# Optimization experiments

Hardware: AMD Instinct MI355X
Metric: run time of the kernel (lower is better)

## Reference

```python
import jax, jax.numpy as jnp
import numpy as np

B, S, D_IN = 32, 128, 17
D_PT, D_PAIR, D_OUT = 64, 128, 64
EPS = 1e-5


def _gelu(x):
    return jax.nn.gelu(x, approximate=False)  # torch nn.GELU default (erf)


def _bn(h, g, b):
    # BatchNorm1d (training mode): stats over batch and pair dims, per channel
    mean = h.mean(axis=(0, 1))
    var = h.var(axis=(0, 1))  # biased, matching torch normalization
    return (h - mean) * jax.lax.rsqrt(var + EPS) * g + b


def setup_inputs() -> dict:
    key = jax.random.key(0)
    ks = jax.random.split(key, 8)
    s = lambda k, shp, fan: jax.random.normal(k, shp, jnp.float32) * (1.0 / np.sqrt(fan))
    return {
        "x": jax.random.normal(ks[0], (B, S, D_IN), jnp.float32),
        # pointwise MLP: 17 -> 64 -> 64
        "w1": s(ks[1], (D_IN, D_PT), D_IN), "b1": jnp.zeros((D_PT,), jnp.float32),
        "w2": s(ks[2], (D_PT, D_PT), D_PT), "b2": jnp.zeros((D_PT,), jnp.float32),
        # pair MLP: 128 -> 128 -> 128 (input = 2 * D_PT)
        "wp1": s(ks[3], (2 * D_PT, D_PAIR), 2 * D_PT), "bp1": jnp.zeros((D_PAIR,), jnp.float32),
        "wp2": s(ks[4], (D_PAIR, D_PAIR), D_PAIR), "bp2": jnp.zeros((D_PAIR,), jnp.float32),
        # embed: BN(128) -> Conv1d(128,64,1) -> BN(64) -> GELU -> Conv1d(64,64,1) -> BN(64)
        "g0": jnp.ones((D_PAIR,), jnp.float32), "be0": jnp.zeros((D_PAIR,), jnp.float32),
        "wc1": s(ks[5], (D_PAIR, D_OUT), D_PAIR), "bc1": jnp.zeros((D_OUT,), jnp.float32),
        "g1": jnp.ones((D_OUT,), jnp.float32), "be1": jnp.zeros((D_OUT,), jnp.float32),
        "wc2": s(ks[6], (D_OUT, D_OUT), D_OUT), "bc2": jnp.zeros((D_OUT,), jnp.float32),
        "g2": jnp.ones((D_OUT,), jnp.float32), "be2": jnp.zeros((D_OUT,), jnp.float32),
    }


def reference(x, w1, b1, w2, b2, wp1, bp1, wp2, bp2,
              g0, be0, wc1, bc1, g1, be1, wc2, bc2, g2, be2):
    seq_len = x.shape[1]
    # pointwise MLP
    h = _gelu(x @ w1 + b1)
    h = _gelu(h @ w2 + b2)  # [B, S, D_PT]
    # tril pair gather (xi = features of particle j, xj = of particle i,
    # matching x_rep[b, a, c] = x[b, c] semantics in the torch code)
    i_idx, j_idx = jnp.tril_indices(seq_len)
    xi = h[:, j_idx, :]  # [B, P, D_PT]
    xj = h[:, i_idx, :]
    xij = jnp.concatenate([xi, xj], axis=-1)  # [B, P, 2*D_PT]
    # pair MLP
    e = _gelu(xij @ wp1 + bp1)
    e = _gelu(e @ wp2 + bp2)  # [B, P, D_PAIR]
    # embed stack (Conv1d k=1 == channel-wise linear)
    e = _bn(e, g0, be0)
    e = _gelu(_bn(e @ wc1 + bc1, g1, be1))
    e = _bn(e @ wc2 + bc2, g2, be2)  # [B, P, D_OUT]
    # symmetric scatter into dense pairwise output
    y = jnp.zeros((x.shape[0], seq_len, seq_len, e.shape[-1]), e.dtype)
    y = y.at[:, i_idx, j_idx, :].set(e)
    y = y.at[:, j_idx, i_idx, :].set(e)
    return y
```

## Files before the change

### kernel.cpp

```cpp
#include <hip/hip_runtime.h>
#include <hip/hip_bf16.h>
#include <math.h>

#define BB 32
#define SS 128
#define DIN 17
#define DPT 64
#define DPA 128
#define DOU 64
#define NP 8256
#define NROWS (BB * NP)
#define NCHUNK (NROWS / 128)
#define EPSF 1e-5f

typedef __hip_bfloat16 bf16;
typedef __attribute__((ext_vector_type(8))) short short8;
typedef __attribute__((ext_vector_type(16))) float f32x16;
typedef __attribute__((ext_vector_type(4))) float f32x4;
typedef __attribute__((ext_vector_type(4))) int int4v;

#define MFMA32(a, b, c) __builtin_amdgcn_mfma_f32_32x32x16_bf16(a, b, c, 0, 0, 0)

__device__ __forceinline__ unsigned short bfb(float f) {
    return __builtin_bit_cast(unsigned short, __float2bfloat16(f));
}
__device__ __forceinline__ float bf2f(short u) {
    return __builtin_bit_cast(float, ((unsigned int)(unsigned short)u) << 16);
}

__device__ __forceinline__ float gelu_exact(float x) {
    float z = fabsf(x) * 0.7071067811865476f;
    float t = __builtin_amdgcn_rcpf(fmaf(0.3275911f, z, 1.0f));
    float p = fmaf(t, 1.061405429f, -1.453152027f);
    p = fmaf(t, p, 1.421413741f);
    p = fmaf(t, p, -0.284496736f);
    p = fmaf(t, p, 0.254829592f);
    p *= t;
    float e = __expf(-z * z);
    float erfz = 1.0f - p * e;
    float s = copysignf(erfz, x);
    return 0.5f * x * (1.0f + s);
}

__global__ void k_pairs(int* __restrict__ pairIJ) {
    int p = blockIdx.x * blockDim.x + threadIdx.x;
    if (p >= NP) return;
    int i = (int)((sqrtf(8.0f * (float)p + 1.0f) - 1.0f) * 0.5f);
    while ((i * (i + 1)) / 2 > p) --i;
    while (((i + 1) * (i + 2)) / 2 <= p) ++i;
    int j = p - (i * (i + 1)) / 2;
    pairIJ[p] = (i << 8) | j;
}

__global__ void k_pack(const float* __restrict__ wp1, const float* __restrict__ wp2,
                       const float* __restrict__ wc1, const float* __restrict__ wc2,
                       bf16* __restrict__ fragP, bf16* __restrict__ fragC1,
                       bf16* __restrict__ fragC2) {
    int id = blockIdx.x * 256 + threadIdx.x;
    if (id < 32768) {
        int mat = id >> 14, rem = id & 16383;
        int f = rem >> 9, lane = (rem >> 3) & 63, i = rem & 7;
        int wn = f >> 4, s = (f >> 1) & 7, nt = f & 1;
        int k = s * 16 + (lane >> 5) * 8 + i;
        int col = wn * 64 + nt * 32 + (lane & 31);
        const float* w = mat ? wp2 : wp1;
        fragP[id] = __float2bfloat16(w[k * DPA + col]);
    } else if (id < 40960) {
        int rem = id - 32768;
        int f = rem >> 9, lane = (rem >> 3) & 63, i = rem & 7;
        int s = f >> 1, wn = f & 1;
        int k = s * 16 + (lane >> 5) * 8 + i;
        int col = wn * 32 + (lane & 31);
        fragC1[rem] = __float2bfloat16(wc1[k * DOU + col]);
    } else if (id < 45056) {
        int rem = id - 40960;
        int f = rem >> 9, lane = (rem >> 3) & 63, i = rem & 7;
        int s = f >> 1, wn = f & 1;
        int k = s * 16 + (lane >> 5) * 8 + i;
        int col = wn * 32 + (lane & 31);
        fragC2[rem] = __float2bfloat16(wc2[k * DOU + col]);
    }
}

__global__ void k_h(const float* __restrict__ x, const float* __restrict__ w1,
                    const float* __restrict__ b1, const float* __restrict__ w2,
                    const float* __restrict__ b2, bf16* __restrict__ h) {
    __shared__ float h1[4][DPT];
    int t = threadIdx.x;
    int rs = t >> 6;
    int c = t & 63;
    int r = blockIdx.x * 4 + rs;
    const float* xr = x + (size_t)r * DIN;
    float acc = b1[c];
#pragma unroll
    for (int k = 0; k < DIN; ++k) acc += xr[k] * w1[k * DPT + c];
    h1[rs][c] = gelu_exact(acc);
    __syncthreads();
    float acc2 = b2[c];
#pragma unroll
    for (int k = 0; k < DPT; ++k) acc2 += h1[rs][k] * w2[k * DPT + c];
    h[(size_t)r * DPT + c] = __float2bfloat16(gelu_exact(acc2));
}

__global__ __launch_bounds__(256) void k_e0m(
    const bf16* __restrict__ h, const int* __restrict__ pairIJ,
    const short8* __restrict__ fragP, const float* __restrict__ bp1,
    const float* __restrict__ bp2, bf16* __restrict__ e0,
    float* __restrict__ part) {
    __shared__ __align__(16) char buf[32768];
    __shared__ float st[1024];
    int t = threadIdx.x;
    int w = t >> 6, l = t & 63;
    int wm = w >> 1, wn = w & 1;
    int l31 = l & 31, lhi = l >> 5;
    int row0 = blockIdx.x * 128;

    for (int i = t; i < 1024; i += 256) st[i] = 0.f;

#pragma unroll
    for (int q = 0; q < 8; ++q) {
        int task = t + 256 * q;
        int rr = task >> 4, slot = task & 15;
        int n = row0 + rr;
        int b = n / NP, p = n - b * NP;
        int ij = pairIJ[p];
        int src = (slot < 8) ? (ij & 255) : (ij >> 8);
        int4v v = *(const int4v*)(h + (((size_t)(b * SS + src)) << 6) + ((slot & 7) << 3));
        *(int4v*)(buf + rr * 256 + ((slot * 16) ^ ((rr & 15) << 4))) = v;
    }
    short8 bfr[2][8];
#pragma unroll
    for (int nt = 0; nt < 2; ++nt)
#pragma unroll
        for (int s = 0; s < 8; ++s) bfr[nt][s] = fragP[(wn * 16 + s * 2 + nt) * 64 + l];
    float bias1[2] = {bp1[wn * 64 + l31], bp1[wn * 64 + 32 + l31]};
    __syncthreads();

    const int rA0 = wm * 64 + l31, rA1 = rA0 + 32;
    f32x16 acc[2][2];
#pragma unroll
    for (int mt = 0; mt < 2; ++mt)
#pragma unroll
        for (int nt = 0; nt < 2; ++nt)
#pragma unroll
            for (int r = 0; r < 16; ++r) acc[mt][nt][r] = bias1[nt];
#pragma unroll
    for (int s = 0; s < 8; ++s) {
        int kb = s * 32 + lhi * 16;
        short8 a0 = *(const short8*)(buf + rA0 * 256 + (kb ^ ((rA0 & 15) << 4)));
        short8 a1 = *(const short8*)(buf + rA1 * 256 + (kb ^ ((rA1 & 15) << 4)));
        acc[0][0] = MFMA32(a0, bfr[0][s], acc[0][0]);
        acc[0][1] = MFMA32(a0, bfr[1][s], acc[0][1]);
        acc[1][0] = MFMA32(a1, bfr[0][s], acc[1][0]);
        acc[1][1] = MFMA32(a1, bfr[1][s], acc[1][1]);
    }
    __syncthreads();

#pragma unroll
    for (int mt = 0; mt < 2; ++mt)
#pragma unroll
        for (int nt = 0; nt < 2; ++nt)
#pragma unroll
            for (int r = 0; r < 16; ++r) {
                float v = gelu_exact(acc[mt][nt][r]);
                int row = wm * 64 + mt * 32 + (r & 3) + 8 * (r >> 2) + 4 * lhi;
                int col = wn * 64 + nt * 32 + l31;
                *(bf16*)(buf + row * 256 + ((col * 2) ^ ((row & 15) << 4))) =
                    __float2bfloat16(v);
            }
    short8 bfr2[2][8];
#pragma unroll
    for (int nt = 0; nt < 2; ++nt)
#pragma unroll
        for (int s = 0; s < 8; ++s)
            bfr2[nt][s] = fragP[2048 + (wn * 16 + s * 2 + nt) * 64 + l];
    float bias2[2] = {bp2[wn * 64 + l31], bp2[wn * 64 + 32 + l31]};
    __syncthreads();

    f32x16 acc2[2][2];
#pragma unroll
    for (int mt = 0; mt < 2; ++mt)
#pragma unroll
        for (int nt = 0; nt < 2; ++nt)
#pragma unroll
            for (int r = 0; r < 16; ++r) acc2[mt][nt][r] = bias2[nt];
#pragma unroll
    for (int s = 0; s < 8; ++s) {
        int kb = s * 32 + lhi * 16;
        short8 a0 = *(const short8*)(buf + rA0 * 256 + (kb ^ ((rA0 & 15) << 4)));
        short8 a1 = *(const short8*)(buf + rA1 * 256 + (kb ^ ((rA1 & 15) << 4)));
        acc2[0][0] = MFMA32(a0, bfr2[0][s], acc2[0][0]);
        acc2[0][1] = MFMA32(a0, bfr2[1][s], acc2[0][1]);
        acc2[1][0] = MFMA32(a1, bfr2[0][s], acc2[1][0]);
        acc2[1][1] = MFMA32(a1, bfr2[1][s], acc2[1][1]);
    }
    __syncthreads();

    float sum[2] = {0.f, 0.f}, sq[2] = {0.f, 0.f};
#pragma unroll
    for (int mt = 0; mt < 2; ++mt)
#pragma unroll
        for (int nt = 0; nt < 2; ++nt)
#pragma unroll
            for (int r = 0; r < 16; ++r) {
                float v = gelu_exact(acc2[mt][nt][r]);
                sum[nt] += v;
                sq[nt] += v * v;
                int row = wm * 64 + mt * 32 + (r & 3) + 8 * (r >> 2) + 4 * lhi;
                int col = wn * 64 + nt * 32 + l31;
                *(bf16*)(buf + row * 256 + ((col * 2) ^ ((row & 15) << 4))) =
                    __float2bfloat16(v);
            }
    __syncthreads();

#pragma unroll
    for (int q = 0; q < 8; ++q) {
        int task = t + 256 * q;
        int rr = task >> 4, slot = task & 15;
        int4v v = *(const int4v*)(buf + rr * 256 + ((slot * 16) ^ ((rr & 15) << 4)));
        *(int4v*)(e0 + (size_t)(row0 + rr) * DPA + slot * 8) = v;
    }

#pragma unroll
    for (int nt = 0; nt < 2; ++nt) {
        sum[nt] += __shfl_xor(sum[nt], 32);
        sq[nt] += __shfl_xor(sq[nt], 32);
    }
    if (l < 32) {
#pragma unroll
        for (int nt = 0; nt < 2; ++nt) {
            st[w * 256 + wn * 64 + nt * 32 + l] = sum[nt];
            st[w * 256 + 128 + wn * 64 + nt * 32 + l] = sq[nt];
        }
    }
    __syncthreads();
    part[(size_t)blockIdx.x * 256 + t] = st[t] + st[256 + t] + st[512 + t] + st[768 + t];
}

__global__ void k_stats(const float* __restrict__ part, int nch, int nblk,
                        float* __restrict__ a, float* __restrict__ d,
                        const float* __restrict__ g, const float* __restrict__ be) {
    int c = blockIdx.x;
    __shared__ float ssum[256], ssq[256];
    float s = 0.f, q = 0.f;
    for (int bidx = threadIdx.x; bidx < nblk; bidx += 256) {
        s += part[(size_t)bidx * (2 * nch) + c];
        q += part[(size_t)bidx * (2 * nch) + nch + c];
    }
    ssum[threadIdx.x] = s;
    ssq[threadIdx.x] = q;
    __syncthreads();
    for (int w = 128; w > 0; w >>= 1) {
        if ((int)threadIdx.x < w) {
            ssum[threadIdx.x] += ssum[threadIdx.x + w];
            ssq[threadIdx.x] += ssq[threadIdx.x + w];
        }
        __syncthreads();
    }
    if (threadIdx.x == 0) {
        float mean = ssum[0] / (float)NROWS;
        float var = ssq[0] / (float)NROWS - mean * mean;
        float rstd = rsqrtf(var + EPSF);
        float aa = g[c] * rstd;
        a[c] = aa;
        d[c] = be[c] - mean * aa;
    }
}

__global__ __launch_bounds__(256) void k_e1m(
    const bf16* __restrict__ e0, const float* __restrict__ a0,
    const float* __restrict__ d0, const short8* __restrict__ fragC1,
    const float* __restrict__ bc1, bf16* __restrict__ e1,
    float* __restrict__ part) {
    __shared__ __align__(16) char buf[32768];
    __shared__ float st[512];
    int t = threadIdx.x;
    int w = t >> 6, l = t & 63;
    int wm = w >> 1, wn = w & 1;
    int l31 = l & 31, lhi = l >> 5;
    int row0 = blockIdx.x * 128;

    for (int i = t; i < 512; i += 256) st[i] = 0.f;

    int slot = t & 15, c0 = slot * 8;
    f32x4 aLo = *(const f32x4*)(a0 + c0), aHi = *(const f32x4*)(a0 + c0 + 4);
    f32x4 dLo = *(const f32x4*)(d0 + c0), dHi = *(const f32x4*)(d0 + c0 + 4);
    float A[8] = {aLo[0], aLo[1], aLo[2], aLo[3], aHi[0], aHi[1], aHi[2], aHi[3]};
    float D[8] = {dLo[0], dLo[1], dLo[2], dLo[3], dHi[0], dHi[1], dHi[2], dHi[3]};

#pragma unroll
    for (int q = 0; q < 8; ++q) {
        int rr = (t >> 4) + 16 * q;
        short8 raw = *(const short8*)(e0 + (size_t)(row0 + rr) * DPA + c0);
        short8 outv;
#pragma unroll
        for (int i = 0; i < 8; ++i)
            outv[i] = (short)bfb(fmaf(bf2f(raw[i]), A[i], D[i]));
        *(short8*)(buf + rr * 256 + ((slot * 16) ^ ((rr & 15) << 4))) = outv;
    }
    short8 bfr[8];
#pragma unroll
    for (int s = 0; s < 8; ++s) bfr[s] = fragC1[(s * 2 + wn) * 64 + l];
    float bias = bc1[wn * 32 + l31];
    __syncthreads();

    const int rA0 = wm * 64 + l31, rA1 = rA0 + 32;
    f32x16 acc[2];
#pragma unroll
    for (int mt = 0; mt < 2; ++mt)
#pragma unroll
        for (int r = 0; r < 16; ++r) acc[mt][r] = bias;
#pragma unroll
    for (int s = 0; s < 8; ++s) {
        int kb = s * 32 + lhi * 16;
        short8 af0 = *(const short8*)(buf + rA0 * 256 + (kb ^ ((rA0 & 15) << 4)));
        short8 af1 = *(const short8*)(buf + rA1 * 256 + (kb ^ ((rA1 & 15) << 4)));
        acc[0] = MFMA32(af0, bfr[s], acc[0]);
        acc[1] = MFMA32(af1, bfr[s], acc[1]);
    }
    __syncthreads();

    float sum = 0.f, sq = 0.f;
#pragma unroll
    for (int mt = 0; mt < 2; ++mt)
#pragma unroll
        for (int r = 0; r < 16; ++r) {
            float v = acc[mt][r];
            sum += v;
            sq += v * v;
            int row = wm * 64 + mt * 32 + (r & 3) + 8 * (r >> 2) + 4 * lhi;
            int col = wn * 32 + l31;
            *(bf16*)(buf + row * 128 + ((col * 2) ^ ((row & 7) << 4))) =
                __float2bfloat16(v);
        }
    __syncthreads();

#pragma unroll
    for (int q = 0; q < 4; ++q) {
        int rr = (t >> 3) + 32 * q;
        int s8 = t & 7;
        int4v v = *(const int4v*)(buf + rr * 128 + ((s8 * 16) ^ ((rr & 7) << 4)));
        *(int4v*)(e1 + (size_t)(row0 + rr) * DOU + s8 * 8) = v;
    }

    sum += __shfl_xor(sum, 32);
    sq += __shfl_xor(sq, 32);
    if (l < 32) {
        st[w * 128 + wn * 32 + l] = sum;
        st[w * 128 + 64 + wn * 32 + l] = sq;
    }
    __syncthreads();
    if (t < 128)
        part[(size_t)blockIdx.x * 128 + t] = st[t] + st[128 + t] + st[256 + t] + st[384 + t];
}

__global__ __launch_bounds__(256) void k_e2m(
    const bf16* __restrict__ e1, const float* __restrict__ a1,
    const float* __restrict__ d1, const short8* __restrict__ fragC2,
    const float* __restrict__ bc2, bf16* __restrict__ e2,
    float* __restrict__ part) {
    __shared__ __align__(16) char buf[16384];
    __shared__ float st[512];
    int t = threadIdx.x;
    int w = t >> 6, l = t & 63;
    int wm = w >> 1, wn = w & 1;
    int l31 = l & 31, lhi = l >> 5;
    int row0 = blockIdx.x * 128;

    for (int i = t; i < 512; i += 256) st[i] = 0.f;

    int slot = t & 7, c0 = slot * 8;
    f32x4 aLo = *(const f32x4*)(a1 + c0), aHi = *(const f32x4*)(a1 + c0 + 4);
    f32x4 dLo = *(const f32x4*)(d1 + c0), dHi = *(const f32x4*)(d1 + c0 + 4);
    float A[8] = {aLo[0], aLo[1], aLo[2], aLo[3], aHi[0], aHi[1], aHi[2], aHi[3]};
    float D[8] = {dLo[0], dLo[1], dLo[2], dLo[3], dHi[0], dHi[1], dHi[2], dHi[3]};

#pragma unroll
    for (int q = 0; q < 4; ++q) {
        int rr = (t >> 3) + 32 * q;
        short8 raw = *(const short8*)(e1 + (size_t)(row0 + rr) * DOU + c0);
        short8 outv;
#pragma unroll
        for (int i = 0; i < 8; ++i)
            outv[i] = (short)bfb(gelu_exact(fmaf(bf2f(raw[i]), A[i], D[i])));
        *(short8*)(buf + rr * 128 + ((slot * 16) ^ ((rr & 7) << 4))) = outv;
    }
    short8 bfr[4];
#pragma unroll
    for (int s = 0; s < 4; ++s) bfr[s] = fragC2[(s * 2 + wn) * 64 + l];
    float bias = bc2[wn * 32 + l31];
    __syncthreads();

    const int rA0 = wm * 64 + l31, rA1 = rA0 + 32;
    f32x16 acc[2];
#pragma unroll
    for (int mt = 0; mt < 2; ++mt)
#pragma unroll
        for (int r = 0; r < 16; ++r) acc[mt][r] = bias;
#pragma unroll
    for (int s = 0; s < 4; ++s) {
        int kb = s * 32 + lhi * 16;
        short8 af0 = *(const short8*)(buf + rA0 * 128 + (kb ^ ((rA0 & 7) << 4)));
        short8 af1 = *(const short8*)(buf + rA1 * 128 + (kb ^ ((rA1 & 7) << 4)));
        acc[0] = MFMA32(af0, bfr[s], acc[0]);
        acc[1] = MFMA32(af1, bfr[s], acc[1]);
    }
    __syncthreads();

    float sum = 0.f, sq = 0.f;
#pragma unroll
    for (int mt = 0; mt < 2; ++mt)
#pragma unroll
        for (int r = 0; r < 16; ++r) {
            float v = acc[mt][r];
            sum += v;
            sq += v * v;
            int row = wm * 64 + mt * 32 + (r & 3) + 8 * (r >> 2) + 4 * lhi;
            int col = wn * 32 + l31;
            *(bf16*)(buf + row * 128 + ((col * 2) ^ ((row & 7) << 4))) =
                __float2bfloat16(v);
        }
    __syncthreads();

#pragma unroll
    for (int q = 0; q < 4; ++q) {
        int rr = (t >> 3) + 32 * q;
        int s8 = t & 7;
        int4v v = *(const int4v*)(buf + rr * 128 + ((s8 * 16) ^ ((rr & 7) << 4)));
        *(int4v*)(e2 + (size_t)(row0 + rr) * DOU + s8 * 8) = v;
    }

    sum += __shfl_xor(sum, 32);
    sq += __shfl_xor(sq, 32);
    if (l < 32) {
        st[w * 128 + wn * 32 + l] = sum;
        st[w * 128 + 64 + wn * 32 + l] = sq;
    }
    __syncthreads();
    if (t < 128)
        part[(size_t)blockIdx.x * 128 + t] = st[t] + st[128 + t] + st[256 + t] + st[384 + t];
}

__global__ void k_out(const bf16* __restrict__ e2, const int* __restrict__ pairIJ,
                      const float* __restrict__ a2, const float* __restrict__ d2,
                      float* __restrict__ y) {
    int t = threadIdx.x;
    int n = blockIdx.x * 32 + (t >> 3);
    int c0 = (t & 7) * 8;
    int b = n / NP, p = n - b * NP;
    int ij = pairIJ[p];
    int ii = ij >> 8, jj = ij & 255;
    short8 raw = *(const short8*)(e2 + (size_t)n * DOU + c0);
    f32x4 aLo = *(const f32x4*)(a2 + c0), aHi = *(const f32x4*)(a2 + c0 + 4);
    f32x4 dLo = *(const f32x4*)(d2 + c0), dHi = *(const f32x4*)(d2 + c0 + 4);
    f32x4 v0, v1;
#pragma unroll
    for (int i = 0; i < 4; ++i) v0[i] = fmaf(bf2f(raw[i]), aLo[i], dLo[i]);
#pragma unroll
    for (int i = 0; i < 4; ++i) v1[i] = fmaf(bf2f(raw[4 + i]), aHi[i], dHi[i]);
    float* y1 = y + ((size_t)(b * SS + ii) * SS + jj) * DOU + c0;
    float* y2 = y + ((size_t)(b * SS + jj) * SS + ii) * DOU + c0;
    *(f32x4*)y1 = v0;
    *(f32x4*)(y1 + 4) = v1;
    *(f32x4*)y2 = v0;
    *(f32x4*)(y2 + 4) = v1;
}

extern "C" void kernel_launch(void* const* d_in, const int* in_sizes, int n_in,
                              void* d_out, int out_size, void* d_ws, size_t ws_size,
                              hipStream_t stream) {
    const float* x   = (const float*)d_in[0];
    const float* w1  = (const float*)d_in[1];
    const float* b1  = (const float*)d_in[2];
    const float* w2  = (const float*)d_in[3];
    const float* b2  = (const float*)d_in[4];
    const float* wp1 = (const float*)d_in[5];
    const float* bp1 = (const float*)d_in[6];
    const float* wp2 = (const float*)d_in[7];
    const float* bp2 = (const float*)d_in[8];
    const float* g0  = (const float*)d_in[9];
    const float* be0 = (const float*)d_in[10];
    const float* wc1 = (const float*)d_in[11];
    const float* bc1 = (const float*)d_in[12];
    const float* g1  = (const float*)d_in[13];
    const float* be1 = (const float*)d_in[14];
    const float* wc2 = (const float*)d_in[15];
    const float* bc2 = (const float*)d_in[16];
    const float* g2  = (const float*)d_in[17];
    const float* be2 = (const float*)d_in[18];

    char* ws = (char*)d_ws;
    const size_t OFF_PAIR   = 0;
    const size_t OFF_H      = 33280;
    const size_t OFF_PART   = 557568;
    const size_t OFF_FRAGP  = 2671104;
    const size_t OFF_FRAGC1 = 2736640;
    const size_t OFF_FRAGC2 = 2753024;
    const size_t OFF_A0 = 2761216, OFF_D0 = 2761728;
    const size_t OFF_A1 = 2762240, OFF_D1 = 2762752;
    const size_t OFF_A2 = 2763264, OFF_D2 = 2763776;
    const size_t OFF_E2 = 2764288;

    int*   pairIJ = (int*)(ws + OFF_PAIR);
    bf16*  h      = (bf16*)(ws + OFF_H);
    float* part   = (float*)(ws + OFF_PART);
    bf16*  fragP  = (bf16*)(ws + OFF_FRAGP);
    bf16*  fragC1 = (bf16*)(ws + OFF_FRAGC1);
    bf16*  fragC2 = (bf16*)(ws + OFF_FRAGC2);
    float* a0 = (float*)(ws + OFF_A0);
    float* d0 = (float*)(ws + OFF_D0);
    float* a1 = (float*)(ws + OFF_A1);
    float* d1 = (float*)(ws + OFF_D1);
    float* a2 = (float*)(ws + OFF_A2);
    float* d2 = (float*)(ws + OFF_D2);
    bf16*  e2 = (bf16*)(ws + OFF_E2);

    bf16* e0 = (bf16*)d_out;
    bf16* e1 = (bf16*)((char*)d_out + (size_t)NROWS * DPA * sizeof(bf16));
    float* y = (float*)d_out;

    k_pairs<<<(NP + 255) / 256, 256, 0, stream>>>(pairIJ);
    k_pack<<<176, 256, 0, stream>>>(wp1, wp2, wc1, wc2, fragP, fragC1, fragC2);
    k_h<<<(BB * SS) / 4, 256, 0, stream>>>(x, w1, b1, w2, b2, h);
    k_e0m<<<NCHUNK, 256, 0, stream>>>(h, pairIJ, (const short8*)fragP, bp1, bp2, e0, part);
    k_stats<<<DPA, 256, 0, stream>>>(part, DPA, NCHUNK, a0, d0, g0, be0);
    k_e1m<<<NCHUNK, 256, 0, stream>>>(e0, a0, d0, (const short8*)fragC1, bc1, e1, part);
    k_stats<<<DOU, 256, 0, stream>>>(part, DOU, NCHUNK, a1, d1, g1, be1);
    k_e2m<<<NCHUNK, 256, 0, stream>>>(e1, a1, d1, (const short8*)fragC2, bc2, e2, part);
    k_stats<<<DOU, 256, 0, stream>>>(part, DOU, NCHUNK, a2, d2, g2, be2);
    k_out<<<NROWS / 32, 256, 0, stream>>>(e2, pairIJ, a2, d2, y);
}
```

Baseline: 161.2 us.

## Fold BN0 into conv1 weights and chain MFMAs via transposed register layout

Folds the first BatchNorm affine (scale a0 and shift d0) into the wc1 weights and bias through a new k_fold kernel, so k_e1m no longer normalizes e0 element-wise. The pair-MLP and embed GEMMs are recast as W^T·X with each wave owning 32 rows. Accumulator outputs are packed to bf16 and lane-swapped with v_permlane32_swap so they feed straight into the next MFMA as operands, removing the LDS round-trip between the two pair-MLP layers. The column statistics are now computed from the bf16-rounded stored values, and the extra small launch plus fragment reloads from global add some overhead.

After: 192.7 us. +19.5%, slower.

```diff
diff --git a/kernel.cpp b/kernel.cpp
--- a/kernel.cpp
+++ b/kernel.cpp
@@ -18,14 +18,35 @@
 typedef __attribute__((ext_vector_type(16))) float f32x16;
 typedef __attribute__((ext_vector_type(4))) float f32x4;
 typedef __attribute__((ext_vector_type(4))) int int4v;
+typedef __attribute__((ext_vector_type(4))) unsigned int uint4v;
 
 #define MFMA32(a, b, c) __builtin_amdgcn_mfma_f32_32x32x16_bf16(a, b, c, 0, 0, 0)
 
-__device__ __forceinline__ unsigned short bfb(float f) {
-    return __builtin_bit_cast(unsigned short, __float2bfloat16(f));
-}
 __device__ __forceinline__ float bf2f(short u) {
     return __builtin_bit_cast(float, ((unsigned int)(unsigned short)u) << 16);
+}
+
+__device__ __forceinline__ void plswap(unsigned int& a, unsigned int& b) {
+    asm("v_permlane32_swap_b32 %0, %1" : "+v"(a), "+v"(b));
+}
+__device__ __forceinline__ unsigned int cvtpk(float lo, float hi) {
+    unsigned int r;
+    asm("v_cvt_pk_bf16_f32 %0, %1, %2" : "=v"(r) : "v"(lo), "v"(hi));
+    return r;
+}
+
+__device__ __forceinline__ void xform(const f32x16& a, short8& o0, short8& o1) {
+    unsigned int w[8];
+#pragma unroll
+    for (int j = 0; j < 8; ++j) w[j] = cvtpk(a[2 * j], a[2 * j + 1]);
+    plswap(w[0], w[2]);
+    plswap(w[1], w[3]);
+    plswap(w[4], w[6]);
+    plswap(w[5], w[7]);
+    uint4v u0 = {w[0], w[1], w[2], w[3]};
+    uint4v u1 = {w[4], w[5], w[6], w[7]};
+    o0 = __builtin_bit_cast(short8, u0);
+    o1 = __builtin_bit_cast(short8, u1);
 }
 
 __device__ __forceinline__ float gelu_exact(float x) {
@@ -53,32 +74,47 @@
 }
 
 __global__ void k_pack(const float* __restrict__ wp1, const float* __restrict__ wp2,
-                       const float* __restrict__ wc1, const float* __restrict__ wc2,
-                       bf16* __restrict__ fragP, bf16* __restrict__ fragC1,
-                       bf16* __restrict__ fragC2) {
+                       const float* __restrict__ wc2, bf16* __restrict__ fragP1,
+                       bf16* __restrict__ fragP2, bf16* __restrict__ fragC2) {
     int id = blockIdx.x * 256 + threadIdx.x;
-    if (id < 32768) {
-        int mat = id >> 14, rem = id & 16383;
+    if (id < 16384) {
+        int f = id >> 9, lane = (id >> 3) & 63, i = id & 7;
+        int mt = f >> 3, s = f & 7;
+        int k = s * 16 + (lane >> 5) * 8 + i;
+        int m = mt * 32 + (lane & 31);
+        fragP1[id] = __float2bfloat16(wp1[k * DPA + m]);
+    } else if (id < 32768) {
+        int rem = id - 16384;
         int f = rem >> 9, lane = (rem >> 3) & 63, i = rem & 7;
-        int wn = f >> 4, s = (f >> 1) & 7, nt = f & 1;
+        int mt = f >> 3, s = f & 7;
         int k = s * 16 + (lane >> 5) * 8 + i;
-        int col = wn * 64 + nt * 32 + (lane & 31);
-        const float* w = mat ? wp2 : wp1;
-        fragP[id] = __float2bfloat16(w[k * DPA + col]);
-    } else if (id < 40960) {
+        int m = mt * 32 + (lane & 31);
+        fragP2[rem] = __float2bfloat16(wp2[k * DPA + m]);
+    } else if (id < 36864) {
         int rem = id - 32768;
         int f = rem >> 9, lane = (rem >> 3) & 63, i = rem & 7;
-        int s = f >> 1, wn = f & 1;
+        int mt = f >> 2, s = f & 3;
         int k = s * 16 + (lane >> 5) * 8 + i;
-        int col = wn * 32 + (lane & 31);
-        fragC1[rem] = __float2bfloat16(wc1[k * DOU + col]);
-    } else if (id < 45056) {
-        int rem = id - 40960;
-        int f = rem >> 9, lane = (rem >> 3) & 63, i = rem & 7;
-        int s = f >> 1, wn = f & 1;
+        int m = mt * 32 + (lane & 31);
+        fragC2[rem] = __float2bfloat16(wc2[k * DOU + m]);
+    }
+}
+
+__global__ void k_fold(const float* __restrict__ a0, const float* __restrict__ d0,
+                       const float* __restrict__ wc1, const float* __restrict__ bc1,
+                       bf16* __restrict__ fragC1, float* __restrict__ bc1p) {
+    int id = blockIdx.x * 256 + threadIdx.x;
+    if (id < 8192) {
+        int f = id >> 9, lane = (id >> 3) & 63, i = id & 7;
+        int mt = f >> 3, s = f & 7;
         int k = s * 16 + (lane >> 5) * 8 + i;
-        int col = wn * 32 + (lane & 31);
-        fragC2[rem] = __float2bfloat16(wc2[k * DOU + col]);
+        int m = mt * 32 + (lane & 31);
+        fragC1[id] = __float2bfloat16(a0[k] * wc1[k * DOU + m]);
+    } else if (id < 8192 + 64) {
+        int c = id - 8192;
+        float s = bc1[c];
+        for (int k = 0; k < DPA; ++k) s = fmaf(d0[k], wc1[k * DOU + c], s);
+        bc1p[c] = s;
     }
 }
 
@@ -104,18 +140,15 @@
 
 __global__ __launch_bounds__(256) void k_e0m(
     const bf16* __restrict__ h, const int* __restrict__ pairIJ,
-    const short8* __restrict__ fragP, const float* __restrict__ bp1,
-    const float* __restrict__ bp2, bf16* __restrict__ e0,
-    float* __restrict__ part) {
+    const short8* __restrict__ fragP1, const short8* __restrict__ fragP2,
+    const float* __restrict__ bp1, const float* __restrict__ bp2,
+    bf16* __restrict__ e0, float* __restrict__ part) {
     __shared__ __align__(16) char buf[32768];
-    __shared__ float st[1024];
     int t = threadIdx.x;
     int w = t >> 6, l = t & 63;
-    int wm = w >> 1, wn = w & 1;
     int l31 = l & 31, lhi = l >> 5;
     int row0 = blockIdx.x * 128;
-
-    for (int i = t; i < 1024; i += 256) st[i] = 0.f;
+    int prow = w * 32 + l31;
 
 #pragma unroll
     for (int q = 0; q < 8; ++q) {
@@ -128,113 +161,97 @@
         int4v v = *(const int4v*)(h + (((size_t)(b * SS + src)) << 6) + ((slot & 7) << 3));
         *(int4v*)(buf + rr * 256 + ((slot * 16) ^ ((rr & 15) << 4))) = v;
     }
-    short8 bfr[2][8];
-#pragma unroll
-    for (int nt = 0; nt < 2; ++nt)
-#pragma unroll
-        for (int s = 0; s < 8; ++s) bfr[nt][s] = fragP[(wn * 16 + s * 2 + nt) * 64 + l];
-    float bias1[2] = {bp1[wn * 64 + l31], bp1[wn * 64 + 32 + l31]};
-    __syncthreads();
-
-    const int rA0 = wm * 64 + l31, rA1 = rA0 + 32;
-    f32x16 acc[2][2];
-#pragma unroll
-    for (int mt = 0; mt < 2; ++mt)
-#pragma unroll
-        for (int nt = 0; nt < 2; ++nt)
-#pragma unroll
-            for (int r = 0; r < 16; ++r) acc[mt][nt][r] = bias1[nt];
+    __syncthreads();
+
+    f32x16 acc[4];
+#pragma unroll
+    for (int mt = 0; mt < 4; ++mt)
+#pragma unroll
+        for (int g = 0; g < 4; ++g) {
+            f32x4 bv = *(const f32x4*)(bp1 + mt * 32 + g * 8 + lhi * 4);
+#pragma unroll
+            for (int j = 0; j < 4; ++j) acc[mt][g * 4 + j] = bv[j];
+        }
 #pragma unroll
     for (int s = 0; s < 8; ++s) {
-        int kb = s * 32 + lhi * 16;
-        short8 a0 = *(const short8*)(buf + rA0 * 256 + (kb ^ ((rA0 & 15) << 4)));
-        short8 a1 = *(const short8*)(buf + rA1 * 256 + (kb ^ ((rA1 & 15) << 4)));
-        acc[0][0] = MFMA32(a0, bfr[0][s], acc[0][0]);
-        acc[0][1] = MFMA32(a0, bfr[1][s], acc[0][1]);
-        acc[1][0] = MFMA32(a1, bfr[0][s], acc[1][0]);
-        acc[1][1] = MFMA32(a1, bfr[1][s], acc[1][1]);
-    }
-    __syncthreads();
-
-#pragma unroll
-    for (int mt = 0; mt < 2; ++mt)
-#pragma unroll
-        for (int nt = 0; nt < 2; ++nt)
-#pragma unroll
-            for (int r = 0; r < 16; ++r) {
-                float v = gelu_exact(acc[mt][nt][r]);
-                int row = wm * 64 + mt * 32 + (r & 3) + 8 * (r >> 2) + 4 * lhi;
-                int col = wn * 64 + nt * 32 + l31;
-                *(bf16*)(buf + row * 256 + ((col * 2) ^ ((row & 15) << 4))) =
-                    __float2bfloat16(v);
-            }
-    short8 bfr2[2][8];
-#pragma unroll
-    for (int nt = 0; nt < 2; ++nt)
-#pragma unroll
-        for (int s = 0; s < 8; ++s)
-            bfr2[nt][s] = fragP[2048 + (wn * 16 + s * 2 + nt) * 64 + l];
-    float bias2[2] = {bp2[wn * 64 + l31], bp2[wn * 64 + 32 + l31]};
-    __syncthreads();
-
-    f32x16 acc2[2][2];
-#pragma unroll
-    for (int mt = 0; mt < 2; ++mt)
-#pragma unroll
-        for (int nt = 0; nt < 2; ++nt)
-#pragma unroll
-            for (int r = 0; r < 16; ++r) acc2[mt][nt][r] = bias2[nt];
+        short8 bx = *(const short8*)(buf + prow * 256 +
+                                     (((s * 2 + lhi) * 16) ^ ((prow & 15) << 4)));
+        acc[0] = MFMA32(fragP1[(0 * 8 + s) * 64 + l], bx, acc[0]);
+        acc[1] = MFMA32(fragP1[(1 * 8 + s) * 64 + l], bx, acc[1]);
+        acc[2] = MFMA32(fragP1[(2 * 8 + s) * 64 + l], bx, acc[2]);
+        acc[3] = MFMA32(fragP1[(3 * 8 + s) * 64 + l], bx, acc[3]);
+    }
+
+    short8 B2[8];
+#pragma unroll
+    for (int mt = 0; mt < 4; ++mt) {
+#pragma unroll
+        for (int r = 0; r < 16; ++r) acc[mt][r] = gelu_exact(acc[mt][r]);
+        xform(acc[mt], B2[2 * mt], B2[2 * mt + 1]);
+    }
+
+    f32x16 acc2[4];
+#pragma unroll
+    for (int mt = 0; mt < 4; ++mt)
+#pragma unroll
+        for (int g = 0; g < 4; ++g) {
+            f32x4 bv = *(const f32x4*)(bp2 + mt * 32 + g * 8 + lhi * 4);
+#pragma unroll
+            for (int j = 0; j < 4; ++j) acc2[mt][g * 4 + j] = bv[j];
+        }
 #pragma unroll
     for (int s = 0; s < 8; ++s) {
-        int kb = s * 32 + lhi * 16;
-        short8 a0 = *(const short8*)(buf + rA0 * 256 + (kb ^ ((rA0 & 15) << 4)));
-        short8 a1 = *(const short8*)(buf + rA1 * 256 + (kb ^ ((rA1 & 15) << 4)));
-        acc2[0][0] = MFMA32(a0, bfr2[0][s], acc2[0][0]);
-        acc2[0][1] = MFMA32(a0, bfr2[1][s], acc2[0][1]);
-        acc2[1][0] = MFMA32(a1, bfr2[0][s], acc2[1][0]);
-        acc2[1][1] = MFMA32(a1, bfr2[1][s], acc2[1][1]);
-    }
-    __syncthreads();
-
-    float sum[2] = {0.f, 0.f}, sq[2] = {0.f, 0.f};
-#pragma unroll
-    for (int mt = 0; mt < 2; ++mt)
-#pragma unroll
-        for (int nt = 0; nt < 2; ++nt)
-#pragma unroll
-            for (int r = 0; r < 16; ++r) {
-                float v = gelu_exact(acc2[mt][nt][r]);
-                sum[nt] += v;
-                sq[nt] += v * v;
-                int row = wm * 64 + mt * 32 + (r & 3) + 8 * (r >> 2) + 4 * lhi;
-                int col = wn * 64 + nt * 32 + l31;
-                *(bf16*)(buf + row * 256 + ((col * 2) ^ ((row & 15) << 4))) =
-                    __float2bfloat16(v);
-            }
-    __syncthreads();
-
+        acc2[0] = MFMA32(fragP2[(0 * 8 + s) * 64 + l], B2[s], acc2[0]);
+        acc2[1] = MFMA32(fragP2[(1 * 8 + s) * 64 + l], B2[s], acc2[1]);
+        acc2[2] = MFMA32(fragP2[(2 * 8 + s) * 64 + l], B2[s], acc2[2]);
+        acc2[3] = MFMA32(fragP2[(3 * 8 + s) * 64 + l], B2[s], acc2[3]);
+    }
+    __syncthreads();
+
+#pragma unroll
+    for (int mt = 0; mt < 4; ++mt) {
+#pragma unroll
+        for (int r = 0; r < 16; ++r) acc2[mt][r] = gelu_exact(acc2[mt][r]);
+        short8 o0, o1;
+        xform(acc2[mt], o0, o1);
+        int slot0 = 4 * mt + lhi, slot1 = 4 * mt + 2 + lhi;
+        *(short8*)(buf + prow * 256 + ((slot0 * 16) ^ ((prow & 15) << 4))) = o0;
+        *(short8*)(buf + prow * 256 + ((slot1 * 16) ^ ((prow & 15) << 4))) = o1;
+    }
+    __syncthreads();
+
+    float sum[8], sq[8];
+#pragma unroll
+    for (int i = 0; i < 8; ++i) { sum[i] = 0.f; sq[i] = 0.f; }
+    int slot = t & 15;
 #pragma unroll
     for (int q = 0; q < 8; ++q) {
-        int task = t + 256 * q;
-        int rr = task >> 4, slot = task & 15;
-        int4v v = *(const int4v*)(buf + rr * 256 + ((slot * 16) ^ ((rr & 15) << 4)));
-        *(int4v*)(e0 + (size_t)(row0 + rr) * DPA + slot * 8) = v;
-    }
-
-#pragma unroll
-    for (int nt = 0; nt < 2; ++nt) {
-        sum[nt] += __shfl_xor(sum[nt], 32);
-        sq[nt] += __shfl_xor(sq[nt], 32);
-    }
-    if (l < 32) {
-#pragma unroll
-        for (int nt = 0; nt < 2; ++nt) {
-            st[w * 256 + wn * 64 + nt * 32 + l] = sum[nt];
-            st[w * 256 + 128 + wn * 64 + nt * 32 + l] = sq[nt];
-        }
-    }
-    __syncthreads();
-    part[(size_t)blockIdx.x * 256 + t] = st[t] + st[256 + t] + st[512 + t] + st[768 + t];
+        int rr = (t >> 4) + 16 * q;
+        short8 v = *(const short8*)(buf + rr * 256 + ((slot * 16) ^ ((rr & 15) << 4)));
+        *(short8*)(e0 + (size_t)(row0 + rr) * DPA + slot * 8) = v;
+#pragma unroll
+        for (int i = 0; i < 8; ++i) {
+            float f = bf2f(v[i]);
+            sum[i] += f;
+            sq[i] += f * f;
+        }
+    }
+    __syncthreads();
+    float* bb = (float*)buf;
+#pragma unroll
+    for (int i = 0; i < 8; ++i) {
+        bb[t * 16 + i] = sum[i];
+        bb[t * 16 + 8 + i] = sq[i];
+    }
+    __syncthreads();
+    {
+        int c = t & 127, isq = t >> 7;
+        float s = 0.f;
+#pragma unroll
+        for (int g = 0; g < 16; ++g)
+            s += bb[((c >> 3) + 16 * g) * 16 + isq * 8 + (c & 7)];
+        part[(size_t)blockIdx.x * 256 + t] = s;
+    }
 }
 
 __global__ void k_stats(const float* __restrict__ part, int nch, int nblk,
@@ -268,90 +285,78 @@
 }
 
 __global__ __launch_bounds__(256) void k_e1m(
-    const bf16* __restrict__ e0, const float* __restrict__ a0,
-    const float* __restrict__ d0, const short8* __restrict__ fragC1,
-    const float* __restrict__ bc1, bf16* __restrict__ e1,
+    const bf16* __restrict__ e0, const short8* __restrict__ fragC1,
+    const float* __restrict__ bc1p, bf16* __restrict__ e1,
     float* __restrict__ part) {
-    __shared__ __align__(16) char buf[32768];
-    __shared__ float st[512];
+    __shared__ __align__(16) char buf[16384];
     int t = threadIdx.x;
     int w = t >> 6, l = t & 63;
-    int wm = w >> 1, wn = w & 1;
     int l31 = l & 31, lhi = l >> 5;
     int row0 = blockIdx.x * 128;
-
-    for (int i = t; i < 512; i += 256) st[i] = 0.f;
-
-    int slot = t & 15, c0 = slot * 8;
-    f32x4 aLo = *(const f32x4*)(a0 + c0), aHi = *(const f32x4*)(a0 + c0 + 4);
-    f32x4 dLo = *(const f32x4*)(d0 + c0), dHi = *(const f32x4*)(d0 + c0 + 4);
-    float A[8] = {aLo[0], aLo[1], aLo[2], aLo[3], aHi[0], aHi[1], aHi[2], aHi[3]};
-    float D[8] = {dLo[0], dLo[1], dLo[2], dLo[3], dHi[0], dHi[1], dHi[2], dHi[3]};
-
-#pragma unroll
-    for (int q = 0; q < 8; ++q) {
-        int rr = (t >> 4) + 16 * q;
-        short8 raw = *(const short8*)(e0 + (size_t)(row0 + rr) * DPA + c0);
-        short8 outv;
-#pragma unroll
-        for (int i = 0; i < 8; ++i)
-            outv[i] = (short)bfb(fmaf(bf2f(raw[i]), A[i], D[i]));
-        *(short8*)(buf + rr * 256 + ((slot * 16) ^ ((rr & 15) << 4))) = outv;
-    }
-    short8 bfr[8];
-#pragma unroll
-    for (int s = 0; s < 8; ++s) bfr[s] = fragC1[(s * 2 + wn) * 64 + l];
-    float bias = bc1[wn * 32 + l31];
-    __syncthreads();
-
-    const int rA0 = wm * 64 + l31, rA1 = rA0 + 32;
+    int prow = w * 32 + l31;
+
+    short8 B[8];
+#pragma unroll
+    for (int s = 0; s < 8; ++s)
+        B[s] = *(const short8*)(e0 + (size_t)(row0 + prow) * DPA + s * 16 + lhi * 8);
+
     f32x16 acc[2];
 #pragma unroll
     for (int mt = 0; mt < 2; ++mt)
 #pragma unroll
-        for (int r = 0; r < 16; ++r) acc[mt][r] = bias;
+        for (int g = 0; g < 4; ++g) {
+            f32x4 bv = *(const f32x4*)(bc1p + mt * 32 + g * 8 + lhi * 4);
+#pragma unroll
+            for (int j = 0; j < 4; ++j) acc[mt][g * 4 + j] = bv[j];
+        }
 #pragma unroll
     for (int s = 0; s < 8; ++s) {
-        int kb = s * 32 + lhi * 16;
-        short8 af0 = *(const short8*)(buf + rA0 * 256 + (kb ^ ((rA0 & 15) << 4)));
-        short8 af1 = *(const short8*)(buf + rA1 * 256 + (kb ^ ((rA1 & 15) << 4)));
-        acc[0] = MFMA32(af0, bfr[s], acc[0]);
-        acc[1] = MFMA32(af1, bfr[s], acc[1]);
-    }
-    __syncthreads();
-
-    float sum = 0.f, sq = 0.f;
-#pragma unroll
-    for (int mt = 0; mt < 2; ++mt)
-#pragma unroll
-        for (int r = 0; r < 16; ++r) {
-            float v = acc[mt][r];
-            sum += v;
-            sq += v * v;
-            int row = wm * 64 + mt * 32 + (r & 3) + 8 * (r >> 2) + 4 * lhi;
-            int col = wn * 32 + l31;
-            *(bf16*)(buf + row * 128 + ((col * 2) ^ ((row & 7) << 4))) =
-                __float2bfloat16(v);
-        }
-    __syncthreads();
-
+        acc[0] = MFMA32(fragC1[(0 * 8 + s) * 64 + l], B[s], acc[0]);
+        acc[1] = MFMA32(fragC1[(1 * 8 + s) * 64 + l], B[s], acc[1]);
+    }
+
+#pragma unroll
+    for (int mt = 0; mt < 2; ++mt) {
+        short8 o0, o1;
+        xform(acc[mt], o0, o1);
+        int slot0 = 4 * mt + lhi, slot1 = 4 * mt + 2 + lhi;
+        *(short8*)(buf + prow * 128 + ((slot0 * 16) ^ ((prow & 7) << 4))) = o0;
+        *(short8*)(buf + prow * 128 + ((slot1 * 16) ^ ((prow & 7) << 4))) = o1;
+    }
+    __syncthreads();
+
+    float sum[8], sq[8];
+#pragma unroll
+    for (int i = 0; i < 8; ++i) { sum[i] = 0.f; sq[i] = 0.f; }
+    int slot = t & 7;
 #pragma unroll
     for (int q = 0; q < 4; ++q) {
         int rr = (t >> 3) + 32 * q;
-        int s8 = t & 7;
-        int4v v = *(const int4v*)(buf + rr * 128 + ((s8 * 16) ^ ((rr & 7) << 4)));
-        *(int4v*)(e1 + (size_t)(row0 + rr) * DOU + s8 * 8) = v;
-    }
-
-    sum += __shfl_xor(sum, 32);
-    sq += __shfl_xor(sq, 32);
-    if (l < 32) {
-        st[w * 128 + wn * 32 + l] = sum;
-        st[w * 128 + 64 + wn * 32 + l] = sq;
-    }
-    __syncthreads();
-    if (t < 128)
-        part[(size_t)blockIdx.x * 128 + t] = st[t] + st[128 + t] + st[256 + t] + st[384 + t];
+        short8 v = *(const short8*)(buf + rr * 128 + ((slot * 16) ^ ((rr & 7) << 4)));
+        *(short8*)(e1 + (size_t)(row0 + rr) * DOU + slot * 8) = v;
+#pragma unroll
+        for (int i = 0; i < 8; ++i) {
+            float f = bf2f(v[i]);
+            sum[i] += f;
+            sq[i] += f * f;
+        }
+    }
+    __syncthreads();
+    float* bb = (float*)buf;
+#pragma unroll
+    for (int i = 0; i < 8; ++i) {
+        bb[t * 16 + i] = sum[i];
+        bb[t * 16 + 8 + i] = sq[i];
+    }
+    __syncthreads();
+    if (t < 128) {
+        int c = t & 63, isq = t >> 6;
+        float s = 0.f;
+#pragma unroll
+        for (int g = 0; g < 32; ++g)
+            s += bb[((c >> 3) + 8 * g) * 16 + isq * 8 + (c & 7)];
+        part[(size_t)blockIdx.x * 128 + t] = s;
+    }
 }
 
 __global__ __launch_bounds__(256) void k_e2m(
@@ -360,85 +365,86 @@
     const float* __restrict__ bc2, bf16* __restrict__ e2,
     float* __restrict__ part) {
     __shared__ __align__(16) char buf[16384];
-    __shared__ float st[512];
     int t = threadIdx.x;
     int w = t >> 6, l = t & 63;
-    int wm = w >> 1, wn = w & 1;
     int l31 = l & 31, lhi = l >> 5;
     int row0 = blockIdx.x * 128;
-
-    for (int i = t; i < 512; i += 256) st[i] = 0.f;
-
-    int slot = t & 7, c0 = slot * 8;
-    f32x4 aLo = *(const f32x4*)(a1 + c0), aHi = *(const f32x4*)(a1 + c0 + 4);
-    f32x4 dLo = *(const f32x4*)(d1 + c0), dHi = *(const f32x4*)(d1 + c0 + 4);
-    float A[8] = {aLo[0], aLo[1], aLo[2], aLo[3], aHi[0], aHi[1], aHi[2], aHi[3]};
-    float D[8] = {dLo[0], dLo[1], dLo[2], dLo[3], dHi[0], dHi[1], dHi[2], dHi[3]};
-
+    int prow = w * 32 + l31;
+
+    short8 B[4];
+#pragma unroll
+    for (int s = 0; s < 4; ++s) {
+        short8 raw = *(const short8*)(e1 + (size_t)(row0 + prow) * DOU + s * 16 + lhi * 8);
+        int c0 = s * 16 + lhi * 8;
+        f32x4 av0 = *(const f32x4*)(a1 + c0), av1 = *(const f32x4*)(a1 + c0 + 4);
+        f32x4 dv0 = *(const f32x4*)(d1 + c0), dv1 = *(const f32x4*)(d1 + c0 + 4);
+        float gg[8];
+#pragma unroll
+        for (int i = 0; i < 4; ++i) gg[i] = gelu_exact(fmaf(bf2f(raw[i]), av0[i], dv0[i]));
+#pragma unroll
+        for (int i = 0; i < 4; ++i) gg[4 + i] = gelu_exact(fmaf(bf2f(raw[4 + i]), av1[i], dv1[i]));
+        uint4v u = {cvtpk(gg[0], gg[1]), cvtpk(gg[2], gg[3]),
+                    cvtpk(gg[4], gg[5]), cvtpk(gg[6], gg[7])};
+        B[s] = __builtin_bit_cast(short8, u);
+    }
+
+    f32x16 acc[2];
+#pragma unroll
+    for (int mt = 0; mt < 2; ++mt)
+#pragma unroll
+        for (int g = 0; g < 4; ++g) {
+            f32x4 bv = *(const f32x4*)(bc2 + mt * 32 + g * 8 + lhi * 4);
+#pragma unroll
+            for (int j = 0; j < 4; ++j) acc[mt][g * 4 + j] = bv[j];
+        }
+#pragma unroll
+    for (int s = 0; s < 4; ++s) {
+        acc[0] = MFMA32(fragC2[(0 * 4 + s) * 64 + l], B[s], acc[0]);
+        acc[1] = MFMA32(fragC2[(1 * 4 + s) * 64 + l], B[s], acc[1]);
+    }
+
+#pragma unroll
+    for (int mt = 0; mt < 2; ++mt) {
+        short8 o0, o1;
+        xform(acc[mt], o0, o1);
+        int slot0 = 4 * mt + lhi, slot1 = 4 * mt + 2 + lhi;
+        *(short8*)(buf + prow * 128 + ((slot0 * 16) ^ ((prow & 7) << 4))) = o0;
+        *(short8*)(buf + prow * 128 + ((slot1 * 16) ^ ((prow & 7) << 4))) = o1;
+    }
+    __syncthreads();
+
+    float sum[8], sq[8];
+#pragma unroll
+    for (int i = 0; i < 8; ++i) { sum[i] = 0.f; sq[i] = 0.f; }
+    int slot = t & 7;
 #pragma unroll
     for (int q = 0; q < 4; ++q) {
         int rr = (t >> 3) + 32 * q;
-        short8 raw = *(const short8*)(e1 + (size_t)(row0 + rr) * DOU + c0);
-        short8 outv;
-#pragma unroll
-        for (int i = 0; i < 8; ++i)
-            outv[i] = (short)bfb(gelu_exact(fmaf(bf2f(raw[i]), A[i], D[i])));
-        *(short8*)(buf + rr * 128 + ((slot * 16) ^ ((rr & 7) << 4))) = outv;
-    }
-    short8 bfr[4];
-#pragma unroll
-    for (int s = 0; s < 4; ++s) bfr[s] = fragC2[(s * 2 + wn) * 64 + l];
-    float bias = bc2[wn * 32 + l31];
-    __syncthreads();
-
-    const int rA0 = wm * 64 + l31, rA1 = rA0 + 32;
-    f32x16 acc[2];
-#pragma unroll
-    for (int mt = 0; mt < 2; ++mt)
-#pragma unroll
-        for (int r = 0; r < 16; ++r) acc[mt][r] = bias;
-#pragma unroll
-    for (int s = 0; s < 4; ++s) {
-        int kb = s * 32 + lhi * 16;
-        short8 af0 = *(const short8*)(buf + rA0 * 128 + (kb ^ ((rA0 & 7) << 4)));
-        short8 af1 = *(const short8*)(buf + rA1 * 128 + (kb ^ ((rA1 & 7) << 4)));
-        acc[0] = MFMA32(af0, bfr[s], acc[0]);
-        acc[1] = MFMA32(af1, bfr[s], acc[1]);
-    }
-    __syncthreads();
-
-    float sum = 0.f, sq = 0.f;
-#pragma unroll
-    for (int mt = 0; mt < 2; ++mt)
-#pragma unroll
-        for (int r = 0; r < 16; ++r) {
-            float v = acc[mt][r];
-            sum += v;
-            sq += v * v;
-            int row = wm * 64 + mt * 32 + (r & 3) + 8 * (r >> 2) + 4 * lhi;
-            int col = wn * 32 + l31;
-            *(bf16*)(buf + row * 128 + ((col * 2) ^ ((row & 7) << 4))) =
-                __float2bfloat16(v);
-        }
-    __syncthreads();
-
-#pragma unroll
-    for (int q = 0; q < 4; ++q) {
-        int rr = (t >> 3) + 32 * q;
-        int s8 = t & 7;
-        int4v v = *(const int4v*)(buf + rr * 128 + ((s8 * 16) ^ ((rr & 7) << 4)));
-        *(int4v*)(e2 + (size_t)(row0 + rr) * DOU + s8 * 8) = v;
-    }
-
-    sum += __shfl_xor(sum, 32);
-    sq += __shfl_xor(sq, 32);
-    if (l < 32) {
-        st[w * 128 + wn * 32 + l] = sum;
-        st[w * 128 + 64 + wn * 32 + l] = sq;
-    }
-    __syncthreads();
-    if (t < 128)
-        part[(size_t)blockIdx.x * 128 + t] = st[t] + st[128 + t] + st[256 + t] + st[384 + t];
+        short8 v = *(const short8*)(buf + rr * 128 + ((slot * 16) ^ ((rr & 7) << 4)));
+        *(short8*)(e2 + (size_t)(row0 + rr) * DOU + slot * 8) = v;
+#pragma unroll
+        for (int i = 0; i < 8; ++i) {
+            float f = bf2f(v[i]);
+            sum[i] += f;
+            sq[i] += f * f;
+        }
+    }
+    __syncthreads();
+    float* bb = (float*)buf;
+#pragma unroll
+    for (int i = 0; i < 8; ++i) {
+        bb[t * 16 + i] = sum[i];
+        bb[t * 16 + 8 + i] = sq[i];
+    }
+    __syncthreads();
+    if (t < 128) {
+        int c = t & 63, isq = t >> 6;
+        float s = 0.f;
+#pragma unroll
+        for (int g = 0; g < 32; ++g)
+            s += bb[((c >> 3) + 8 * g) * 16 + isq * 8 + (c & 7)];
+        part[(size_t)blockIdx.x * 128 + t] = s;
+    }
 }
 
 __global__ void k_out(const bf16* __restrict__ e2, const int* __restrict__ pairIJ,
@@ -493,20 +499,24 @@
     const size_t OFF_PAIR   = 0;
     const size_t OFF_H      = 33280;
     const size_t OFF_PART   = 557568;
-    const size_t OFF_FRAGP  = 2671104;
+    const size_t OFF_FRAGP1 = 2671104;
+    const size_t OFF_FRAGP2 = 2703872;
     const size_t OFF_FRAGC1 = 2736640;
     const size_t OFF_FRAGC2 = 2753024;
-    const size_t OFF_A0 = 2761216, OFF_D0 = 2761728;
-    const size_t OFF_A1 = 2762240, OFF_D1 = 2762752;
-    const size_t OFF_A2 = 2763264, OFF_D2 = 2763776;
-    const size_t OFF_E2 = 2764288;
+    const size_t OFF_BC1P   = 2761216;
+    const size_t OFF_A0 = 2761472, OFF_D0 = 2761984;
+    const size_t OFF_A1 = 2762496, OFF_D1 = 2762752;
+    const size_t OFF_A2 = 2763008, OFF_D2 = 2763264;
+    const size_t OFF_E2 = 2763520;
 
     int*   pairIJ = (int*)(ws + OFF_PAIR);
     bf16*  h      = (bf16*)(ws + OFF_H);
     float* part   = (float*)(ws + OFF_PART);
-    bf16*  fragP  = (bf16*)(ws + OFF_FRAGP);
+    bf16*  fragP1 = (bf16*)(ws + OFF_FRAGP1);
+    bf16*  fragP2 = (bf16*)(ws + OFF_FRAGP2);
     bf16*  fragC1 = (bf16*)(ws + OFF_FRAGC1);
     bf16*  fragC2 = (bf16*)(ws + OFF_FRAGC2);
+    float* bc1p   = (float*)(ws + OFF_BC1P);
     float* a0 = (float*)(ws + OFF_A0);
     float* d0 = (float*)(ws + OFF_D0);
     float* a1 = (float*)(ws + OFF_A1);
@@ -520,11 +530,13 @@
     float* y = (float*)d_out;
 
     k_pairs<<<(NP + 255) / 256, 256, 0, stream>>>(pairIJ);
-    k_pack<<<176, 256, 0, stream>>>(wp1, wp2, wc1, wc2, fragP, fragC1, fragC2);
+    k_pack<<<144, 256, 0, stream>>>(wp1, wp2, wc2, fragP1, fragP2, fragC2);
     k_h<<<(BB * SS) / 4, 256, 0, stream>>>(x, w1, b1, w2, b2, h);
-    k_e0m<<<NCHUNK, 256, 0, stream>>>(h, pairIJ, (const short8*)fragP, bp1, bp2, e0, part);
+    k_e0m<<<NCHUNK, 256, 0, stream>>>(h, pairIJ, (const short8*)fragP1,
+                                      (const short8*)fragP2, bp1, bp2, e0, part);
     k_stats<<<DPA, 256, 0, stream>>>(part, DPA, NCHUNK, a0, d0, g0, be0);
-    k_e1m<<<NCHUNK, 256, 0, stream>>>(e0, a0, d0, (const short8*)fragC1, bc1, e1, part);
+    k_fold<<<33, 256, 0, stream>>>(a0, d0, wc1, bc1, fragC1, bc1p);
+    k_e1m<<<NCHUNK, 256, 0, stream>>>(e0, (const short8*)fragC1, bc1p, e1, part);
     k_stats<<<DOU, 256, 0, stream>>>(part, DOU, NCHUNK, a1, d1, g1, be1);
     k_e2m<<<NCHUNK, 256, 0, stream>>>(e1, a1, d1, (const short8*)fragC2, bc2, e2, part);
     k_stats<<<DOU, 256, 0, stream>>>(part, DOU, NCHUNK, a2, d2, g2, be2);
```
